# Kernel optimization log

Hardware: AMD Instinct MI355X
Metric: run time of the kernel (lower is better)

Reference implementation:

```python
import jax, jax.numpy as jnp
import numpy as np

N0, N1, N2 = 100000, 25000, 6250
E0, E1, E2 = 600000, 150000, 40000
K = 6
NUM_CLASSES = 10


def setup_inputs() -> dict:
    key = jax.random.key(0)
    ks = jax.random.split(key, 20)
    inp = {
        "pos": jax.random.normal(ks[0], (N0, 3), dtype=jnp.float32),
        "edge_index0": jax.random.randint(ks[1], (2, E0), 0, N0, dtype=jnp.int32),
        "edge_index1": jax.random.randint(ks[2], (2, E1), 0, N1, dtype=jnp.int32),
        "edge_index2": jax.random.randint(ks[3], (2, E2), 0, N2, dtype=jnp.int32),
        "d0_rows": jax.random.randint(ks[4], (N0,), 0, N1, dtype=jnp.int32),
        "d0_cols": jax.random.randint(ks[5], (N0,), 0, N0, dtype=jnp.int32),
        "d0_vals": jax.random.uniform(ks[6], (N0,), dtype=jnp.float32),
        "d1_rows": jax.random.randint(ks[7], (N1,), 0, N2, dtype=jnp.int32),
        "d1_cols": jax.random.randint(ks[8], (N1,), 0, N1, dtype=jnp.int32),
        "d1_vals": jax.random.uniform(ks[9], (N1,), dtype=jnp.float32),
        "W0": jax.random.normal(ks[10], (K, 3, 32), dtype=jnp.float32) * 0.1,
        "b0": jax.random.normal(ks[11], (32,), dtype=jnp.float32) * 0.1,
        "W1": jax.random.normal(ks[12], (K, 32, 64), dtype=jnp.float32) * 0.1,
        "b1": jax.random.normal(ks[13], (64,), dtype=jnp.float32) * 0.1,
        "W2": jax.random.normal(ks[14], (K, 64, 128), dtype=jnp.float32) * 0.1,
        "b2": jax.random.normal(ks[15], (128,), dtype=jnp.float32) * 0.1,
        "lin_w": jax.random.normal(ks[16], (NUM_CLASSES, N2 * 128), dtype=jnp.float32) * 0.01,
        "lin_b": jax.random.normal(ks[17], (NUM_CLASSES,), dtype=jnp.float32) * 0.1,
    }
    return inp


def _cheb_edge_weights(row, col, n):
    # PyG get_laplacian(sym) followed by 2L/lambda_max - I with lambda_max=2:
    # diagonal becomes 0, off-diagonal weight = -deg^{-1/2}[row] * deg^{-1/2}[col]
    deg = jax.ops.segment_sum(jnp.ones(row.shape[0], jnp.float32), row, num_segments=n)
    dinv = jnp.where(deg > 0, 1.0 / jnp.sqrt(deg), 0.0)
    return -dinv[row] * dinv[col]


def _cheb_conv(x, edge_index, W, b, n):
    # Chebyshev recurrence: Tx0 = x, Tx1 = L_hat x, Tx_k = 2 L_hat Tx_{k-1} - Tx_{k-2}
    row, col = edge_index[0], edge_index[1]
    w = _cheb_edge_weights(row, col, n)

    def prop(z):  # [n, C] -> [n, C] scatter-gather over edges
        return jax.ops.segment_sum(w[:, None] * z[col], row, num_segments=n)

    Tx0 = x
    out = Tx0 @ W[0]
    Tx1 = prop(x)
    out = out + Tx1 @ W[1]
    for k in range(2, W.shape[0]):
        Tx2 = 2.0 * prop(Tx1) - Tx0
        out = out + Tx2 @ W[k]
        Tx0, Tx1 = Tx1, Tx2
    return out + b


def _pool(x, rows, cols, vals, n_out):
    # torch.sparse.mm(D, x) with D given in COO form
    return jax.ops.segment_sum(vals[:, None] * x[cols], rows, num_segments=n_out)


def reference(pos, edge_index0, edge_index1, edge_index2,
              d0_rows, d0_cols, d0_vals, d1_rows, d1_cols, d1_vals,
              W0, b0, W1, b1, W2, b2, lin_w, lin_b):
    x = jax.nn.relu(_cheb_conv(pos, edge_index0, W0, b0, N0))
    x = _pool(x, d0_rows, d0_cols, d0_vals, N1)
    x = jax.nn.relu(_cheb_conv(x, edge_index1, W1, b1, N1))
    x = _pool(x, d1_rows, d1_cols, d1_vals, N2)
    x = _cheb_conv(x, edge_index2, W2, b2, N2)  # no ReLU on last conv
    Z = lin_w @ x.reshape(-1) + lin_b
    return Z
```

## Files before the change

kernel.cpp:

```cpp
#include <hip/hip_runtime.h>


#define TPB 256
#define NB   318
#define BCAP 8192
#define EPB  4096
#define TXS  800000LL

static inline int gs(long long n) { return (int)((n + TPB - 1) / TPB); }

struct Desc5 {
    const int* rows[5];
    const int* cols[5];
    const float* vals[5];
    int eoff[6];
    int doff[5];
};


__global__ void k_binA(Desc5 d, int* __restrict__ gbcnt, int2* __restrict__ binrec,
                       int Etot) {
    __shared__ int2 srec[EPB];
    __shared__ unsigned short sbuck[EPB];
    __shared__ int scnt[NB], sbase[NB], slcur[NB];
    int tid = threadIdx.x;
    int e0 = blockIdx.x * EPB;
    int ne = min(EPB, Etot - e0);
    for (int b = tid; b < NB; b += 256) scnt[b] = 0;
    __syncthreads();
    for (int i = tid; i < ne; i += 256) {
        int e = e0 + i;
        int s = 0;
        while (e >= d.eoff[s + 1]) ++s;
        int le = e - d.eoff[s];
        int grow = d.doff[s] + d.rows[s][le];
        int col = d.cols[s][le];
        int vb = (s >= 3) ? __float_as_int(d.vals[s][le]) : 0;
        int b = grow >> 9;
        srec[i] = make_int2(((grow & 511) << 17) | col, vb);
        sbuck[i] = (unsigned short)b;
        atomicAdd(&scnt[b], 1);
    }
    __syncthreads();
    for (int b = tid; b < NB; b += 256) {
        sbase[b] = scnt[b] > 0 ? atomicAdd(&gbcnt[b], scnt[b]) : 0;
        slcur[b] = 0;
    }
    __syncthreads();
    for (int i = tid; i < ne; i += 256) {
        int b = sbuck[i];
        int off = atomicAdd(&slcur[b], 1);
        binrec[(long long)b * BCAP + sbase[b] + off] = srec[i];
    }
}

__global__ void k_bscan(const int* __restrict__ gbcnt, int* __restrict__ gbbase) {
    int lane = threadIdx.x;
    int carry = 0;
    for (int base = 0; base < NB; base += 64) {
        int i = base + lane;
        int v = (i < NB) ? gbcnt[i] : 0;
        int s = v;
#pragma unroll
        for (int off = 1; off < 64; off <<= 1) {
            int t = __shfl_up(s, off, 64);
            if (lane >= off) s += t;
        }
        if (i < NB) gbbase[i] = carry + s - v;
        carry += __shfl(s, 63, 64);
    }
}


__device__ inline void bucket_count_scan(const int2* __restrict__ br, int ne,
                                         int* cnt, int* lexcl, int* wsum) {
    int tid = threadIdx.x;
    cnt[2 * tid] = 0; cnt[2 * tid + 1] = 0;
    __syncthreads();
    for (int i = tid; i < ne; i += 256)
        atomicAdd(&cnt[br[i].x >> 17], 1);
    __syncthreads();
    int c0 = cnt[2 * tid], c1 = cnt[2 * tid + 1], p = c0 + c1;
    int lane = tid & 63, wid = tid >> 6;
    int s = p;
#pragma unroll
    for (int off = 1; off < 64; off <<= 1) {
        int t = __shfl_up(s, off, 64);
        if (lane >= off) s += t;
    }
    if (lane == 63) wsum[wid] = s;
    __syncthreads();
    int add = 0;
    for (int w = 0; w < wid; ++w) add += wsum[w];
    int ep = add + s - p;
    lexcl[2 * tid] = ep; lexcl[2 * tid + 1] = ep + c0;
    __syncthreads();
}

__global__ void k_B1(const int* __restrict__ gbcnt, const int* __restrict__ gbbase,
                     const int2* __restrict__ binrec, int* __restrict__ rowptr,
                     float* __restrict__ dinv, int ntot, int ndinv, int Etot) {
    __shared__ int cnt[512], lexcl[512], wsum[4];
    int bucket = blockIdx.x, tid = threadIdx.x;
    int ne = gbcnt[bucket];
    const int2* br = binrec + (long long)bucket * BCAP;
    bucket_count_scan(br, ne, cnt, lexcl, wsum);
    int base = gbbase[bucket];
    int row0 = bucket << 9;
    int nrows = min(512, ntot - row0);
    for (int lr = tid; lr < nrows; lr += 256) {
        int grow = row0 + lr;
        rowptr[grow] = base + lexcl[lr];
        if (grow < ndinv) {
            int c = cnt[lr];
            dinv[grow] = c > 0 ? 1.0f / sqrtf((float)c) : 0.f;
        }
    }
    if (bucket == 0 && tid == 0) rowptr[ntot] = Etot;
}

__global__ void k_B2(const int* __restrict__ gbcnt, const int* __restrict__ gbbase,
                     const int2* __restrict__ binrec, const float* __restrict__ dinv,
                     int2* __restrict__ rec) {
    __shared__ int cnt[512], lexcl[512], lcur[512], wsum[4];
    int bucket = blockIdx.x, tid = threadIdx.x;
    int ne = gbcnt[bucket];
    const int2* br = binrec + (long long)bucket * BCAP;
    bucket_count_scan(br, ne, cnt, lexcl, wsum);
    lcur[2 * tid] = 0; lcur[2 * tid + 1] = 0;
    __syncthreads();
    int base = gbbase[bucket];
    int row0 = bucket << 9;
    for (int i = tid; i < ne; i += 256) {
        int2 r = br[i];
        int lr = r.x >> 17, col = r.x & 0x1FFFF;
        int grow = row0 + lr;
        int pos = base + lexcl[lr] + atomicAdd(&lcur[lr], 1);
        float wv;
        if (grow < 100000)      wv = dinv[col];
        else if (grow < 125000) wv = dinv[100000 + col];
        else if (grow < 131250) wv = dinv[125000 + col];
        else                    wv = __int_as_float(r.y);
        rec[pos] = make_int2(col, __float_as_int(wv));
    }
}

__global__ void k_pad4(const float* __restrict__ pos, float4* __restrict__ dst, int n) {
    int i = blockIdx.x * blockDim.x + threadIdx.x;
    if (i < n) dst[i] = make_float4(pos[3 * i], pos[3 * i + 1], pos[3 * i + 2], 0.f);
}


__global__ void k_sprop_c4(const int* __restrict__ rowptr, const int2* __restrict__ rec,
                           const float* __restrict__ dinv, const float* __restrict__ src,
                           const float* __restrict__ prev, float* __restrict__ dst,
                           int n, int mode) {
    int r = blockIdx.x * blockDim.x + threadIdx.x;
    if (r >= n) return;
    int s0 = rowptr[r], s1 = rowptr[r + 1];
    float4 a0 = make_float4(0.f, 0.f, 0.f, 0.f);
    float4 a1 = a0, a2 = a0, a3 = a0;
    int j = s0;
    for (; j + 4 <= s1; j += 4) {
        int2 r0 = rec[j], r1 = rec[j + 1], r2 = rec[j + 2], r3 = rec[j + 3];
        float w0 = __int_as_float(r0.y), w1 = __int_as_float(r1.y);
        float w2 = __int_as_float(r2.y), w3 = __int_as_float(r3.y);
        float4 s0v = *(const float4*)(src + (long long)r0.x * 4);
        float4 s1v = *(const float4*)(src + (long long)r1.x * 4);
        float4 s2v = *(const float4*)(src + (long long)r2.x * 4);
        float4 s3v = *(const float4*)(src + (long long)r3.x * 4);
        a0.x += w0 * s0v.x; a0.y += w0 * s0v.y; a0.z += w0 * s0v.z; a0.w += w0 * s0v.w;
        a1.x += w1 * s1v.x; a1.y += w1 * s1v.y; a1.z += w1 * s1v.z; a1.w += w1 * s1v.w;
        a2.x += w2 * s2v.x; a2.y += w2 * s2v.y; a2.z += w2 * s2v.z; a2.w += w2 * s2v.w;
        a3.x += w3 * s3v.x; a3.y += w3 * s3v.y; a3.z += w3 * s3v.z; a3.w += w3 * s3v.w;
    }
    for (; j < s1; ++j) {
        int2 rr = rec[j];
        float w = __int_as_float(rr.y);
        float4 s = *(const float4*)(src + (long long)rr.x * 4);
        a0.x += w * s.x; a0.y += w * s.y; a0.z += w * s.z; a0.w += w * s.w;
    }
    a0.x += a1.x + a2.x + a3.x; a0.y += a1.y + a2.y + a3.y;
    a0.z += a1.z + a2.z + a3.z; a0.w += a1.w + a2.w + a3.w;
    float m = -dinv[r];
    long long o = (long long)r * 4;
    float4 out;
    if (mode) {
        float4 p = *(const float4*)(prev + o);
        out.x = 2.f * m * a0.x - p.x; out.y = 2.f * m * a0.y - p.y;
        out.z = 2.f * m * a0.z - p.z; out.w = 2.f * m * a0.w - p.w;
    } else {
        out.x = m * a0.x; out.y = m * a0.y; out.z = m * a0.z; out.w = m * a0.w;
    }
    *(float4*)(dst + o) = out;
}

template <int C>
__global__ void k_sprop_t(const int* __restrict__ rowptr, const int2* __restrict__ rec,
                          const float* __restrict__ dinv, const float* __restrict__ src,
                          const float* __restrict__ prev, float* __restrict__ dst,
                          int n, int mode) {
    constexpr int C4 = C / 4;
    int idx = blockIdx.x * blockDim.x + threadIdx.x;
    if (idx >= n * C4) return;
    int r = idx / C4, c4 = (idx - r * C4) * 4;
    int s0 = rowptr[r], s1 = rowptr[r + 1];
    float4 acca = make_float4(0.f, 0.f, 0.f, 0.f);
    float4 accb = make_float4(0.f, 0.f, 0.f, 0.f);
    int j = s0;
    for (; j + 2 <= s1; j += 2) {
        int2 ra = rec[j], rb = rec[j + 1];
        float wa = __int_as_float(ra.y), wb = __int_as_float(rb.y);
        float4 sa = *(const float4*)(src + (long long)ra.x * C + c4);
        float4 sb = *(const float4*)(src + (long long)rb.x * C + c4);
        acca.x += wa * sa.x; acca.y += wa * sa.y; acca.z += wa * sa.z; acca.w += wa * sa.w;
        accb.x += wb * sb.x; accb.y += wb * sb.y; accb.z += wb * sb.z; accb.w += wb * sb.w;
    }
    if (j < s1) {
        int2 rr = rec[j];
        float w = __int_as_float(rr.y);
        float4 s = *(const float4*)(src + (long long)rr.x * C + c4);
        acca.x += w * s.x; acca.y += w * s.y; acca.z += w * s.z; acca.w += w * s.w;
    }
    acca.x += accb.x; acca.y += accb.y; acca.z += accb.z; acca.w += accb.w;
    float m = -dinv[r];
    long long o = (long long)r * C + c4;
    float4 out;
    if (mode) {
        float4 p = *(const float4*)(prev + o);
        out.x = 2.f * m * acca.x - p.x; out.y = 2.f * m * acca.y - p.y;
        out.z = 2.f * m * acca.z - p.z; out.w = 2.f * m * acca.w - p.w;
    } else {
        out.x = m * acca.x; out.y = m * acca.y; out.z = m * acca.z; out.w = m * acca.w;
    }
    *(float4*)(dst + o) = out;
}


template <int C>
__global__ void k_spool4_t(const int* __restrict__ rowptr, const int2* __restrict__ rec,
                           const float* __restrict__ x, float* __restrict__ out, int n) {
    constexpr int C4 = C / 4;
    int idx = blockIdx.x * blockDim.x + threadIdx.x;
    if (idx >= n * C4) return;
    int r = idx / C4, c4 = (idx - r * C4) * 4;
    int s0 = rowptr[r], s1 = rowptr[r + 1];
    float4 acca = make_float4(0.f, 0.f, 0.f, 0.f);
    float4 accb = make_float4(0.f, 0.f, 0.f, 0.f);
    int j = s0;
    for (; j + 2 <= s1; j += 2) {
        int2 ra = rec[j], rb = rec[j + 1];
        float va = __int_as_float(ra.y), vb = __int_as_float(rb.y);
        float4 sa = *(const float4*)(x + (long long)ra.x * C + c4);
        float4 sb = *(const float4*)(x + (long long)rb.x * C + c4);
        acca.x += va * fmaxf(sa.x, 0.f); acca.y += va * fmaxf(sa.y, 0.f);
        acca.z += va * fmaxf(sa.z, 0.f); acca.w += va * fmaxf(sa.w, 0.f);
        accb.x += vb * fmaxf(sb.x, 0.f); accb.y += vb * fmaxf(sb.y, 0.f);
        accb.z += vb * fmaxf(sb.z, 0.f); accb.w += vb * fmaxf(sb.w, 0.f);
    }
    if (j < s1) {
        int2 rr = rec[j];
        float v = __int_as_float(rr.y);
        float4 s = *(const float4*)(x + (long long)rr.x * C + c4);
        acca.x += v * fmaxf(s.x, 0.f); acca.y += v * fmaxf(s.y, 0.f);
        acca.z += v * fmaxf(s.z, 0.f); acca.w += v * fmaxf(s.w, 0.f);
    }
    acca.x += accb.x; acca.y += accb.y; acca.z += accb.z; acca.w += accb.w;
    *(float4*)(out + (long long)r * C + c4) = acca;
}


template <int C, int KSPLIT>
__global__ void k_pool_f(const int* __restrict__ rowptr, const int2* __restrict__ rec,
                         const float* __restrict__ part, const float* __restrict__ bias,
                         float* __restrict__ out, int n, int partStride) {
    constexpr int C4 = C / 4;
    int idx = blockIdx.x * blockDim.x + threadIdx.x;
    if (idx >= n * C4) return;
    int r = idx / C4, c4 = (idx - r * C4) * 4;
    int s0 = rowptr[r], s1 = rowptr[r + 1];
    float4 bb = *(const float4*)(bias + c4);
    float4 acc = make_float4(0.f, 0.f, 0.f, 0.f);
    for (int j = s0; j < s1; ++j) {
        int2 rr = rec[j];
        float v = __int_as_float(rr.y);
        float4 x = bb;
#pragma unroll
        for (int s = 0; s < KSPLIT; ++s) {
            float4 p = *(const float4*)(part + (long long)s * partStride + (long long)rr.x * C + c4);
            x.x += p.x; x.y += p.y; x.z += p.z; x.w += p.w;
        }
        acc.x += v * fmaxf(x.x, 0.f); acc.y += v * fmaxf(x.y, 0.f);
        acc.z += v * fmaxf(x.z, 0.f); acc.w += v * fmaxf(x.w, 0.f);
    }
    *(float4*)(out + (long long)r * C + c4) = acc;
}


__global__ void k_outgemm0(float* __restrict__ out, const float* __restrict__ txbase,
                           const float* __restrict__ W, const float* __restrict__ b,
                           int n) {
    int idx = blockIdx.x * blockDim.x + threadIdx.x;
    if (idx >= n * 8) return;
    int node = idx >> 3, co = (idx & 7) * 4;
    float4 acc = *(const float4*)(b + co);
#pragma unroll
    for (int k = 0; k < 6; ++k) {
        float4 xv = *(const float4*)(txbase + k * TXS + (long long)node * 4);
        const float* Wk = W + k * 96 + co;
        float4 w0 = *(const float4*)(Wk);
        float4 w1 = *(const float4*)(Wk + 32);
        float4 w2 = *(const float4*)(Wk + 64);
        acc.x += xv.x * w0.x + xv.y * w1.x + xv.z * w2.x;
        acc.y += xv.x * w0.y + xv.y * w1.y + xv.z * w2.y;
        acc.z += xv.x * w0.z + xv.y * w1.z + xv.z * w2.z;
        acc.w += xv.x * w0.w + xv.y * w1.w + xv.z * w2.w;
    }
    *(float4*)(out + (long long)node * 32 + co) = acc;
}


template <int CIN, int COUT, int KSPLIT, int NT>
__global__ __launch_bounds__(256, 4)
void k_outsplit4(float* __restrict__ part, const float* __restrict__ txbase,
                 const float* __restrict__ W, int n, int partStride) {
    constexpr int CO4 = COUT / 4;
    constexpr int KPER = 6 / KSPLIT;
    int per = (n / NT) * CO4;
    int idx = blockIdx.x * blockDim.x + threadIdx.x;
    if (idx >= per * KSPLIT) return;
    int s = idx / per, t = idx - s * per;
    int tile = t / CO4, co = (t - tile * CO4) * 4;
    int node0 = tile * NT;
    float4 acc[NT];
#pragma unroll
    for (int i = 0; i < NT; ++i) acc[i] = make_float4(0.f, 0.f, 0.f, 0.f);
#pragma unroll 1
    for (int kk = 0; kk < KPER; ++kk) {
        int k = s * KPER + kk;
        const float* xb = txbase + (long long)k * TXS + (long long)node0 * CIN;
        const float* Wk = W + (long long)k * CIN * COUT + co;
#pragma unroll 1
        for (int c4 = 0; c4 < CIN / 4; ++c4) {
            const float* Wr = Wk + c4 * 4 * COUT;
            float4 w0 = *(const float4*)(Wr);
            float4 w1 = *(const float4*)(Wr + COUT);
            float4 w2 = *(const float4*)(Wr + 2 * COUT);
            float4 w3 = *(const float4*)(Wr + 3 * COUT);
#pragma unroll
            for (int i = 0; i < NT; ++i) {
                float4 xv = *(const float4*)(xb + i * CIN + c4 * 4);
                acc[i].x += xv.x * w0.x + xv.y * w1.x + xv.z * w2.x + xv.w * w3.x;
                acc[i].y += xv.x * w0.y + xv.y * w1.y + xv.z * w2.y + xv.w * w3.y;
                acc[i].z += xv.x * w0.z + xv.y * w1.z + xv.z * w2.z + xv.w * w3.z;
                acc[i].w += xv.x * w0.w + xv.y * w1.w + xv.z * w2.w + xv.w * w3.w;
            }
        }
    }
    float* op = part + (long long)s * partStride + (long long)node0 * COUT + co;
#pragma unroll
    for (int i = 0; i < NT; ++i)
        *(float4*)(op + (long long)i * COUT) = acc[i];
}


__global__ void k_linear_partial_f(const float* __restrict__ lw,
                                   const float4* __restrict__ part,
                                   const float* __restrict__ b2,
                                   float* __restrict__ partials,
                                   int len4, int len, int nblk) {
    float acc[10];
#pragma unroll
    for (int j = 0; j < 10; ++j) acc[j] = 0.f;
    const float4* b2v = (const float4*)b2;
    for (int i = blockIdx.x * blockDim.x + threadIdx.x; i < len4;
         i += gridDim.x * blockDim.x) {
        float4 xv = b2v[i & 31];
#pragma unroll
        for (int s = 0; s < 6; ++s) {
            float4 p = part[s * 200000 + i];
            xv.x += p.x; xv.y += p.y; xv.z += p.z; xv.w += p.w;
        }
#pragma unroll
        for (int j = 0; j < 10; ++j) {
            float4 wv = *(const float4*)(lw + (long long)j * len + i * 4);
            acc[j] += xv.x * wv.x + xv.y * wv.y + xv.z * wv.z + xv.w * wv.w;
        }
    }
    __shared__ float lds[4][10];
    int wid = threadIdx.x >> 6, lane = threadIdx.x & 63;
#pragma unroll
    for (int j = 0; j < 10; ++j) {
        float v = acc[j];
        for (int off = 32; off > 0; off >>= 1) v += __shfl_down(v, off, 64);
        if (lane == 0) lds[wid][j] = v;
    }
    __syncthreads();
    if (threadIdx.x < 10) {
        float s = lds[0][threadIdx.x] + lds[1][threadIdx.x] +
                  lds[2][threadIdx.x] + lds[3][threadIdx.x];
        partials[threadIdx.x * nblk + blockIdx.x] = s;
    }
}

__global__ void k_linear_final(const float* __restrict__ partials,
                               const float* __restrict__ lb,
                               float* __restrict__ out, int nblk) {
    int j = threadIdx.x >> 6, lane = threadIdx.x & 63;
    float v = 0.f;
    for (int b = lane; b < nblk; b += 64) v += partials[j * nblk + b];
    for (int off = 32; off > 0; off >>= 1) v += __shfl_down(v, off, 64);
    if (lane == 0) out[j] = lb[j] + v;
}

extern "C" void kernel_launch(void* const* d_in, const int* in_sizes, int n_in,
                              void* d_out, int out_size, void* d_ws, size_t ws_size,
                              hipStream_t stream) {
    const int cN0 = 100000, cN1 = 25000, cN2 = 6250;
    const int cE0 = 600000, cE1 = 150000, cE2 = 40000;
    const int NBLK = 512;

    const float* pos = (const float*)d_in[0];
    const int*   ei0 = (const int*)d_in[1];
    const int*   ei1 = (const int*)d_in[2];
    const int*   ei2 = (const int*)d_in[3];
    const int*   d0r = (const int*)d_in[4];
    const int*   d0c = (const int*)d_in[5];
    const float* d0v = (const float*)d_in[6];
    const int*   d1r = (const int*)d_in[7];
    const int*   d1c = (const int*)d_in[8];
    const float* d1v = (const float*)d_in[9];
    const float* W0  = (const float*)d_in[10];
    const float* b0  = (const float*)d_in[11];
    const float* W1  = (const float*)d_in[12];
    const float* b1  = (const float*)d_in[13];
    const float* W2  = (const float*)d_in[14];
    const float* b2  = (const float*)d_in[15];
    const float* lw  = (const float*)d_in[16];
    const float* lb  = (const float*)d_in[17];
    float* outZ = (float*)d_out;

    const int ntot = cN0 + cN1 + cN2 + cN1 + cN2;
    const int Etot = cE0 + cE1 + cE2 + cN0 + cN1;
    const int Eg   = cE0 + cE1 + cE2;
    const int ndinv = cN0 + cN1 + cN2;
    const int doff0 = 0, doff1 = cN0, doff2 = cN0 + cN1,
              doffp0 = doff2 + cN2, doffp1 = doffp0 + cN1;

    int*   iws    = (int*)d_ws;
    int*   gbcnt  = iws;
    int*   gbbase = gbcnt + 320;
    int*   rowptr = gbbase + 320;
    float* dinv   = (float*)(rowptr + 162504);
    int2*  binrec = (int2*)(dinv + 131256);
    int2*  rec    = binrec + (long long)NB * BCAP;
    float* txbuf  = (float*)(rec + 915000);
    float* part   = txbuf + 6 * TXS;
    float* bufOut = part + 4800000;
    float* lpart  = bufOut + 3200000;

    Desc5 d;
    d.rows[0] = ei0;        d.cols[0] = ei0 + cE0; d.vals[0] = nullptr;
    d.rows[1] = ei1;        d.cols[1] = ei1 + cE1; d.vals[1] = nullptr;
    d.rows[2] = ei2;        d.cols[2] = ei2 + cE2; d.vals[2] = nullptr;
    d.rows[3] = d0r;        d.cols[3] = d0c;       d.vals[3] = d0v;
    d.rows[4] = d1r;        d.cols[4] = d1c;       d.vals[4] = d1v;
    d.eoff[0] = 0;
    d.eoff[1] = cE0;
    d.eoff[2] = cE0 + cE1;
    d.eoff[3] = Eg;
    d.eoff[4] = Eg + cN0;
    d.eoff[5] = Etot;
    d.doff[0] = doff0; d.doff[1] = doff1; d.doff[2] = doff2;
    d.doff[3] = doffp0; d.doff[4] = doffp1;

    k_pad4<<<gs(cN0), TPB, 0, stream>>>(pos, (float4*)txbuf, cN0);

    hipMemsetAsync(gbcnt, 0, (size_t)NB * 4, stream);
    k_binA<<<(Etot + EPB - 1) / EPB, TPB, 0, stream>>>(d, gbcnt, binrec, Etot);
    k_bscan<<<1, 64, 0, stream>>>(gbcnt, gbbase);
    k_B1<<<NB, TPB, 0, stream>>>(gbcnt, gbbase, binrec, rowptr, dinv, ntot, ndinv, Etot);
    k_B2<<<NB, TPB, 0, stream>>>(gbcnt, gbbase, binrec, dinv, rec);

    auto run_sprops = [&](int doffs, int n, int Cs) {
        const int* rp = rowptr + doffs;
        const float* dv = dinv + doffs;
        auto sprop = [&](int kdst, int mode) {
            const float* src = txbuf + (long long)(kdst - 1) * TXS;
            const float* prev = (kdst >= 2) ? txbuf + (long long)(kdst - 2) * TXS : nullptr;
            float* dst = txbuf + (long long)kdst * TXS;
            long long work = (long long)n * (Cs >> 2);
            if (Cs == 4)
                k_sprop_c4<<<gs(n), TPB, 0, stream>>>(rp, rec, dv, src, prev, dst, n, mode);
            else if (Cs == 32)
                k_sprop_t<32><<<gs(work), TPB, 0, stream>>>(rp, rec, dv, src, prev, dst, n, mode);
            else
                k_sprop_t<64><<<gs(work), TPB, 0, stream>>>(rp, rec, dv, src, prev, dst, n, mode);
        };
        sprop(1, 0);
        for (int k = 2; k < 6; ++k) sprop(k, 1);
    };

    run_sprops(doff0, cN0, 4);
    k_outgemm0<<<gs((long long)cN0 * 8), TPB, 0, stream>>>(bufOut, txbuf, W0, b0, cN0);
    k_spool4_t<32><<<gs((long long)cN1 * 8), TPB, 0, stream>>>(
        rowptr + doffp0, rec, bufOut, txbuf, cN1);

    run_sprops(doff1, cN1, 32);
    {
        const int pstride = cN1 * 64;
        k_outsplit4<32, 64, 3, 4><<<gs((long long)(cN1 / 4) * 16 * 3), TPB, 0, stream>>>(
            part, txbuf, W1, cN1, pstride);
        k_pool_f<64, 3><<<gs((long long)cN2 * 16), TPB, 0, stream>>>(
            rowptr + doffp1, rec, part, b1, txbuf, cN2, pstride);
    }

    run_sprops(doff2, cN2, 64);
    {
        const int pstride = cN2 * 128;
        k_outsplit4<64, 128, 6, 2><<<gs((long long)(cN2 / 2) * 32 * 6), TPB, 0, stream>>>(
            part, txbuf, W2, cN2, pstride);
        k_linear_partial_f<<<NBLK, TPB, 0, stream>>>(
            lw, (const float4*)part, b2, lpart, cN2 * 128 / 4, cN2 * 128, NBLK);
        k_linear_final<<<1, 640, 0, stream>>>(lpart, lb, outZ, NBLK);
    }
}
```

Before: 263.5 us.

## Fuse last level-0 Chebyshev step into output GEMM and vectorize edge record loads

The final level-0 propagation step now runs inside a new fused kernel that also does the per-node 3->32 output GEMM. This removes one launch and the write and re-read of the Tx5 buffer. k_B2 now reads the row pointers computed by k_B1 instead of recounting and rescanning its bucket. The propagate and pool loops align to even edge indices and load two int2 records at once as an int4. The fused kernel has one thread per node loop over all 32 outputs, which lowers parallelism compared with the old 8-threads-per-node GEMM.

```diff
diff --git a/kernel.cpp b/kernel.cpp
--- a/kernel.cpp
+++ b/kernel.cpp
@@ -71,32 +71,6 @@
     }
 }
 
-
-__device__ inline void bucket_count_scan(const int2* __restrict__ br, int ne,
-                                         int* cnt, int* lexcl, int* wsum) {
-    int tid = threadIdx.x;
-    cnt[2 * tid] = 0; cnt[2 * tid + 1] = 0;
-    __syncthreads();
-    for (int i = tid; i < ne; i += 256)
-        atomicAdd(&cnt[br[i].x >> 17], 1);
-    __syncthreads();
-    int c0 = cnt[2 * tid], c1 = cnt[2 * tid + 1], p = c0 + c1;
-    int lane = tid & 63, wid = tid >> 6;
-    int s = p;
-#pragma unroll
-    for (int off = 1; off < 64; off <<= 1) {
-        int t = __shfl_up(s, off, 64);
-        if (lane >= off) s += t;
-    }
-    if (lane == 63) wsum[wid] = s;
-    __syncthreads();
-    int add = 0;
-    for (int w = 0; w < wid; ++w) add += wsum[w];
-    int ep = add + s - p;
-    lexcl[2 * tid] = ep; lexcl[2 * tid + 1] = ep + c0;
-    __syncthreads();
-}
-
 __global__ void k_B1(const int* __restrict__ gbcnt, const int* __restrict__ gbbase,
                      const int2* __restrict__ binrec, int* __restrict__ rowptr,
                      float* __restrict__ dinv, int ntot, int ndinv, int Etot) {
@@ -104,7 +78,26 @@
     int bucket = blockIdx.x, tid = threadIdx.x;
     int ne = gbcnt[bucket];
     const int2* br = binrec + (long long)bucket * BCAP;
-    bucket_count_scan(br, ne, cnt, lexcl, wsum);
+    cnt[2 * tid] = 0; cnt[2 * tid + 1] = 0;
+    __syncthreads();
+    for (int i = tid; i < ne; i += 256)
+        atomicAdd(&cnt[br[i].x >> 17], 1);
+    __syncthreads();
+    int c0 = cnt[2 * tid], c1 = cnt[2 * tid + 1], p = c0 + c1;
+    int lane = tid & 63, wid = tid >> 6;
+    int s = p;
+#pragma unroll
+    for (int off = 1; off < 64; off <<= 1) {
+        int t = __shfl_up(s, off, 64);
+        if (lane >= off) s += t;
+    }
+    if (lane == 63) wsum[wid] = s;
+    __syncthreads();
+    int add = 0;
+    for (int w = 0; w < wid; ++w) add += wsum[w];
+    int ep = add + s - p;
+    lexcl[2 * tid] = ep; lexcl[2 * tid + 1] = ep + c0;
+    __syncthreads();
     int base = gbbase[bucket];
     int row0 = bucket << 9;
     int nrows = min(512, ntot - row0);
@@ -119,23 +112,25 @@
     if (bucket == 0 && tid == 0) rowptr[ntot] = Etot;
 }
 
-__global__ void k_B2(const int* __restrict__ gbcnt, const int* __restrict__ gbbase,
-                     const int2* __restrict__ binrec, const float* __restrict__ dinv,
-                     int2* __restrict__ rec) {
-    __shared__ int cnt[512], lexcl[512], lcur[512], wsum[4];
+__global__ void k_B2(const int* __restrict__ gbcnt, const int2* __restrict__ binrec,
+                     const int* __restrict__ rowptr, const float* __restrict__ dinv,
+                     int2* __restrict__ rec, int ntot) {
+    __shared__ int lbase[512], lcur[512];
     int bucket = blockIdx.x, tid = threadIdx.x;
+    int row0 = bucket << 9;
+    for (int i = tid; i < 512; i += 256) {
+        int grow = row0 + i;
+        lbase[i] = (grow < ntot) ? rowptr[grow] : 0;
+        lcur[i] = 0;
+    }
+    __syncthreads();
     int ne = gbcnt[bucket];
     const int2* br = binrec + (long long)bucket * BCAP;
-    bucket_count_scan(br, ne, cnt, lexcl, wsum);
-    lcur[2 * tid] = 0; lcur[2 * tid + 1] = 0;
-    __syncthreads();
-    int base = gbbase[bucket];
-    int row0 = bucket << 9;
     for (int i = tid; i < ne; i += 256) {
         int2 r = br[i];
         int lr = r.x >> 17, col = r.x & 0x1FFFF;
         int grow = row0 + lr;
-        int pos = base + lexcl[lr] + atomicAdd(&lcur[lr], 1);
+        int pos = lbase[lr] + atomicAdd(&lcur[lr], 1);
         float wv;
         if (grow < 100000)      wv = dinv[col];
         else if (grow < 125000) wv = dinv[100000 + col];
@@ -161,20 +156,37 @@
     float4 a0 = make_float4(0.f, 0.f, 0.f, 0.f);
     float4 a1 = a0, a2 = a0, a3 = a0;
     int j = s0;
+    if ((j & 1) && j < s1) {
+        int2 rr = rec[j];
+        float w = __int_as_float(rr.y);
+        float4 s = *(const float4*)(src + (long long)rr.x * 4);
+        a0.x += w * s.x; a0.y += w * s.y; a0.z += w * s.z; a0.w += w * s.w;
+        ++j;
+    }
     for (; j + 4 <= s1; j += 4) {
-        int2 r0 = rec[j], r1 = rec[j + 1], r2 = rec[j + 2], r3 = rec[j + 3];
-        float w0 = __int_as_float(r0.y), w1 = __int_as_float(r1.y);
-        float w2 = __int_as_float(r2.y), w3 = __int_as_float(r3.y);
-        float4 s0v = *(const float4*)(src + (long long)r0.x * 4);
-        float4 s1v = *(const float4*)(src + (long long)r1.x * 4);
-        float4 s2v = *(const float4*)(src + (long long)r2.x * 4);
-        float4 s3v = *(const float4*)(src + (long long)r3.x * 4);
+        int4 q0 = *(const int4*)(rec + j);
+        int4 q1 = *(const int4*)(rec + j + 2);
+        float w0 = __int_as_float(q0.y), w1 = __int_as_float(q0.w);
+        float w2 = __int_as_float(q1.y), w3 = __int_as_float(q1.w);
+        float4 s0v = *(const float4*)(src + (long long)q0.x * 4);
+        float4 s1v = *(const float4*)(src + (long long)q0.z * 4);
+        float4 s2v = *(const float4*)(src + (long long)q1.x * 4);
+        float4 s3v = *(const float4*)(src + (long long)q1.z * 4);
         a0.x += w0 * s0v.x; a0.y += w0 * s0v.y; a0.z += w0 * s0v.z; a0.w += w0 * s0v.w;
         a1.x += w1 * s1v.x; a1.y += w1 * s1v.y; a1.z += w1 * s1v.z; a1.w += w1 * s1v.w;
         a2.x += w2 * s2v.x; a2.y += w2 * s2v.y; a2.z += w2 * s2v.z; a2.w += w2 * s2v.w;
         a3.x += w3 * s3v.x; a3.y += w3 * s3v.y; a3.z += w3 * s3v.z; a3.w += w3 * s3v.w;
     }
-    for (; j < s1; ++j) {
+    if (j + 2 <= s1) {
+        int4 q = *(const int4*)(rec + j);
+        float wa = __int_as_float(q.y), wb = __int_as_float(q.w);
+        float4 sa = *(const float4*)(src + (long long)q.x * 4);
+        float4 sb = *(const float4*)(src + (long long)q.z * 4);
+        a0.x += wa * sa.x; a0.y += wa * sa.y; a0.z += wa * sa.z; a0.w += wa * sa.w;
+        a1.x += wb * sb.x; a1.y += wb * sb.y; a1.z += wb * sb.z; a1.w += wb * sb.w;
+        j += 2;
+    }
+    if (j < s1) {
         int2 rr = rec[j];
         float w = __int_as_float(rr.y);
         float4 s = *(const float4*)(src + (long long)rr.x * 4);
@@ -193,6 +205,67 @@
         out.x = m * a0.x; out.y = m * a0.y; out.z = m * a0.z; out.w = m * a0.w;
     }
     *(float4*)(dst + o) = out;
+}
+
+__global__ __launch_bounds__(256, 4)
+void k_conv0_final(const int* __restrict__ rowptr, const int2* __restrict__ rec,
+                   const float* __restrict__ dinv, const float* __restrict__ txbase,
+                   const float* __restrict__ W, const float* __restrict__ b,
+                   float* __restrict__ out, int n) {
+    int r = blockIdx.x * blockDim.x + threadIdx.x;
+    if (r >= n) return;
+    const float* src = txbase + 4 * TXS;
+    int s0 = rowptr[r], s1 = rowptr[r + 1];
+    float4 a0 = make_float4(0.f, 0.f, 0.f, 0.f);
+    float4 a1 = a0;
+    int j = s0;
+    if ((j & 1) && j < s1) {
+        int2 rr = rec[j];
+        float w = __int_as_float(rr.y);
+        float4 s = *(const float4*)(src + (long long)rr.x * 4);
+        a0.x += w * s.x; a0.y += w * s.y; a0.z += w * s.z;
+        ++j;
+    }
+    for (; j + 2 <= s1; j += 2) {
+        int4 q = *(const int4*)(rec + j);
+        float wa = __int_as_float(q.y), wb = __int_as_float(q.w);
+        float4 sa = *(const float4*)(src + (long long)q.x * 4);
+        float4 sb = *(const float4*)(src + (long long)q.z * 4);
+        a0.x += wa * sa.x; a0.y += wa * sa.y; a0.z += wa * sa.z;
+        a1.x += wb * sb.x; a1.y += wb * sb.y; a1.z += wb * sb.z;
+    }
+    if (j < s1) {
+        int2 rr = rec[j];
+        float w = __int_as_float(rr.y);
+        float4 s = *(const float4*)(src + (long long)rr.x * 4);
+        a0.x += w * s.x; a0.y += w * s.y; a0.z += w * s.z;
+    }
+    a0.x += a1.x; a0.y += a1.y; a0.z += a1.z;
+    float m = -dinv[r];
+    float4 xv[6];
+#pragma unroll
+    for (int k = 0; k < 5; ++k)
+        xv[k] = *(const float4*)(txbase + (long long)k * TXS + (long long)r * 4);
+    xv[5].x = 2.f * m * a0.x - xv[3].x;
+    xv[5].y = 2.f * m * a0.y - xv[3].y;
+    xv[5].z = 2.f * m * a0.z - xv[3].z;
+    float* op = out + (long long)r * 32;
+#pragma unroll 1
+    for (int co4 = 0; co4 < 8; ++co4) {
+        float4 acc = *(const float4*)(b + co4 * 4);
+#pragma unroll
+        for (int k = 0; k < 6; ++k) {
+            const float* Wk = W + k * 96 + co4 * 4;
+            float4 w0 = *(const float4*)(Wk);
+            float4 w1 = *(const float4*)(Wk + 32);
+            float4 w2 = *(const float4*)(Wk + 64);
+            acc.x += xv[k].x * w0.x + xv[k].y * w1.x + xv[k].z * w2.x;
+            acc.y += xv[k].x * w0.y + xv[k].y * w1.y + xv[k].z * w2.y;
+            acc.z += xv[k].x * w0.z + xv[k].y * w1.z + xv[k].z * w2.z;
+            acc.w += xv[k].x * w0.w + xv[k].y * w1.w + xv[k].z * w2.w;
+        }
+        *(float4*)(op + co4 * 4) = acc;
+    }
 }
 
 template <int C>
@@ -208,11 +281,18 @@
     float4 acca = make_float4(0.f, 0.f, 0.f, 0.f);
     float4 accb = make_float4(0.f, 0.f, 0.f, 0.f);
     int j = s0;
+    if ((j & 1) && j < s1) {
+        int2 rr = rec[j];
+        float w = __int_as_float(rr.y);
+        float4 s = *(const float4*)(src + (long long)rr.x * C + c4);
+        acca.x += w * s.x; acca.y += w * s.y; acca.z += w * s.z; acca.w += w * s.w;
+        ++j;
+    }
     for (; j + 2 <= s1; j += 2) {
-        int2 ra = rec[j], rb = rec[j + 1];
-        float wa = __int_as_float(ra.y), wb = __int_as_float(rb.y);
-        float4 sa = *(const float4*)(src + (long long)ra.x * C + c4);
-        float4 sb = *(const float4*)(src + (long long)rb.x * C + c4);
+        int4 q = *(const int4*)(rec + j);
+        float wa = __int_as_float(q.y), wb = __int_as_float(q.w);
+        float4 sa = *(const float4*)(src + (long long)q.x * C + c4);
+        float4 sb = *(const float4*)(src + (long long)q.z * C + c4);
         acca.x += wa * sa.x; acca.y += wa * sa.y; acca.z += wa * sa.z; acca.w += wa * sa.w;
         accb.x += wb * sb.x; accb.y += wb * sb.y; accb.z += wb * sb.z; accb.w += wb * sb.w;
     }
@@ -248,11 +328,19 @@
     float4 acca = make_float4(0.f, 0.f, 0.f, 0.f);
     float4 accb = make_float4(0.f, 0.f, 0.f, 0.f);
     int j = s0;
+    if ((j & 1) && j < s1) {
+        int2 rr = rec[j];
+        float v = __int_as_float(rr.y);
+        float4 s = *(const float4*)(x + (long long)rr.x * C + c4);
+        acca.x += v * fmaxf(s.x, 0.f); acca.y += v * fmaxf(s.y, 0.f);
+        acca.z += v * fmaxf(s.z, 0.f); acca.w += v * fmaxf(s.w, 0.f);
+        ++j;
+    }
     for (; j + 2 <= s1; j += 2) {
-        int2 ra = rec[j], rb = rec[j + 1];
-        float va = __int_as_float(ra.y), vb = __int_as_float(rb.y);
-        float4 sa = *(const float4*)(x + (long long)ra.x * C + c4);
-        float4 sb = *(const float4*)(x + (long long)rb.x * C + c4);
+        int4 q = *(const int4*)(rec + j);
+        float va = __int_as_float(q.y), vb = __int_as_float(q.w);
+        float4 sa = *(const float4*)(x + (long long)q.x * C + c4);
+        float4 sb = *(const float4*)(x + (long long)q.z * C + c4);
         acca.x += va * fmaxf(sa.x, 0.f); acca.y += va * fmaxf(sa.y, 0.f);
         acca.z += va * fmaxf(sa.z, 0.f); acca.w += va * fmaxf(sa.w, 0.f);
         accb.x += vb * fmaxf(sb.x, 0.f); accb.y += vb * fmaxf(sb.y, 0.f);
@@ -294,29 +382,6 @@
         acc.z += v * fmaxf(x.z, 0.f); acc.w += v * fmaxf(x.w, 0.f);
     }
     *(float4*)(out + (long long)r * C + c4) = acc;
-}
-
-
-__global__ void k_outgemm0(float* __restrict__ out, const float* __restrict__ txbase,
-                           const float* __restrict__ W, const float* __restrict__ b,
-                           int n) {
-    int idx = blockIdx.x * blockDim.x + threadIdx.x;
-    if (idx >= n * 8) return;
-    int node = idx >> 3, co = (idx & 7) * 4;
-    float4 acc = *(const float4*)(b + co);
-#pragma unroll
-    for (int k = 0; k < 6; ++k) {
-        float4 xv = *(const float4*)(txbase + k * TXS + (long long)node * 4);
-        const float* Wk = W + k * 96 + co;
-        float4 w0 = *(const float4*)(Wk);
-        float4 w1 = *(const float4*)(Wk + 32);
-        float4 w2 = *(const float4*)(Wk + 64);
-        acc.x += xv.x * w0.x + xv.y * w1.x + xv.z * w2.x;
-        acc.y += xv.x * w0.y + xv.y * w1.y + xv.z * w2.y;
-        acc.z += xv.x * w0.z + xv.y * w1.z + xv.z * w2.z;
-        acc.w += xv.x * w0.w + xv.y * w1.w + xv.z * w2.w;
-    }
-    *(float4*)(out + (long long)node * 32 + co) = acc;
 }
 
 
@@ -480,9 +545,9 @@
     k_binA<<<(Etot + EPB - 1) / EPB, TPB, 0, stream>>>(d, gbcnt, binrec, Etot);
     k_bscan<<<1, 64, 0, stream>>>(gbcnt, gbbase);
     k_B1<<<NB, TPB, 0, stream>>>(gbcnt, gbbase, binrec, rowptr, dinv, ntot, ndinv, Etot);
-    k_B2<<<NB, TPB, 0, stream>>>(gbcnt, gbbase, binrec, dinv, rec);
-
-    auto run_sprops = [&](int doffs, int n, int Cs) {
+    k_B2<<<NB, TPB, 0, stream>>>(gbcnt, binrec, rowptr, dinv, rec, ntot);
+
+    auto run_sprops = [&](int doffs, int n, int Cs, int kmax) {
         const int* rp = rowptr + doffs;
         const float* dv = dinv + doffs;
         auto sprop = [&](int kdst, int mode) {
@@ -498,15 +563,16 @@
                 k_sprop_t<64><<<gs(work), TPB, 0, stream>>>(rp, rec, dv, src, prev, dst, n, mode);
         };
         sprop(1, 0);
-        for (int k = 2; k < 6; ++k) sprop(k, 1);
+        for (int k = 2; k <= kmax; ++k) sprop(k, 1);
     };
 
-    run_sprops(doff0, cN0, 4);
-    k_outgemm0<<<gs((long long)cN0 * 8), TPB, 0, stream>>>(bufOut, txbuf, W0, b0, cN0);
+    run_sprops(doff0, cN0, 4, 4);
+    k_conv0_final<<<gs(cN0), TPB, 0, stream>>>(
+        rowptr + doff0, rec, dinv + doff0, txbuf, W0, b0, bufOut, cN0);
     k_spool4_t<32><<<gs((long long)cN1 * 8), TPB, 0, stream>>>(
         rowptr + doffp0, rec, bufOut, txbuf, cN1);
 
-    run_sprops(doff1, cN1, 32);
+    run_sprops(doff1, cN1, 32, 5);
     {
         const int pstride = cN1 * 64;
         k_outsplit4<32, 64, 3, 4><<<gs((long long)(cN1 / 4) * 16 * 3), TPB, 0, stream>>>(
@@ -515,7 +581,7 @@
             rowptr + doffp1, rec, part, b1, txbuf, cN2, pstride);
     }
 
-    run_sprops(doff2, cN2, 64);
+    run_sprops(doff2, cN2, 64, 5);
     {
         const int pstride = cN2 * 128;
         k_outsplit4<64, 128, 6, 2><<<gs((long long)(cN2 / 2) * 32 * 6), TPB, 0, stream>>>(
```

Result: slower. 269.0 us (+2.1%).
